# Optimization experiments

Measured on AMD Instinct MI355X. Metric: run time of the kernel, lower is better.

Reference implementation:

```python
import jax, jax.numpy as jnp
import numpy as np

B, S, IN, OUT = 4, 4096, 4096, 4096
N, R = 8, 64  # n_adapters, rank


def setup_inputs() -> dict:
    key = jax.random.key(0)
    ks = jax.random.split(key, 7)
    x = jax.random.normal(ks[0], (B, S, IN), dtype=jnp.float32)
    W = jax.random.normal(ks[1], (OUT, IN), dtype=jnp.float32) * 0.02
    b = jax.random.normal(ks[2], (OUT,), dtype=jnp.float32) * 0.02
    downs = jax.random.normal(ks[3], (N, R, IN), dtype=jnp.float32) * 0.02
    ups = jax.random.normal(ks[4], (N, OUT, R), dtype=jnp.float32) * 0.02
    mags = jax.random.uniform(ks[5], (N, OUT), dtype=jnp.float32)
    scales = jax.random.uniform(ks[6], (N,), dtype=jnp.float32)
    return {"x": x, "W": W, "b": b, "downs": downs, "ups": ups, "mags": mags, "scales": scales}


def reference(x, W, b, downs, ups, mags, scales):
    # Base linear: y = x @ W.T + b
    out = jnp.einsum("bsi,oi->bso", x, W) + b
    # All adapters batched: t[b,s,n,r] = x @ down_n.T
    t = jnp.einsum("bsi,nri->bsnr", x, downs)
    # Fold per-adapter DoRA magnitude and effective scale into the up proj:
    # delta = sum_n sc_n * mag_n * (t_n @ up_n.T)
    up_eff = ups * mags[:, :, None] * scales[:, None, None]  # [N, OUT, R]
    delta = jnp.einsum("bsnr,nor->bso", t, up_eff)
    return out + delta
```

## Files before the change

kernel.cpp:

```cpp
#include <hip/hip_runtime.h>


#define B_DIM 4
#define S_DIM 4096
#define IND   4096
#define OUTD  4096
#define NA    8
#define RK    64
#define MROWS (B_DIM * S_DIM)
#define KADAPT (NA * RK)

typedef __attribute__((ext_vector_type(8))) short short8;
typedef __attribute__((ext_vector_type(8))) unsigned short ushort8;
typedef __attribute__((ext_vector_type(4))) float float4v;

__device__ __forceinline__ unsigned short f2bf(float f) {
  unsigned int u = __builtin_bit_cast(unsigned int, f);
  u += 0x7FFFu + ((u >> 16) & 1u);
  return (unsigned short)(u >> 16);
}

__global__ void fold_up_k(const float* __restrict__ ups, const float* __restrict__ mags,
                          const float* __restrict__ scales, unsigned short* __restrict__ up_eff) {
  int tid = blockIdx.x * 256 + threadIdx.x;
  int o  = tid >> 9;
  int nr = tid & 511;
  int n  = nr >> 6;
  int r  = nr & 63;
  float v = ups[((size_t)n * OUTD + o) * RK + r] * mags[n * OUTD + o] * scales[n];
  up_eff[tid] = f2bf(v);
}

__global__ void tdown_k(const float* __restrict__ downs, unsigned short* __restrict__ dT) {
  int tid = blockIdx.x * 256 + threadIdx.x;
  int i  = tid >> 9;
  int nr = tid & 511;
  dT[tid] = f2bf(downs[(size_t)nr * IND + i]);
}

__global__ void cvt_x_k(const float* __restrict__ x, unsigned short* __restrict__ xb) {
  int tid = blockIdx.x * 256 + threadIdx.x;
  const float4v* xv = (const float4v*)x;
  float4v a = xv[2 * tid];
  float4v b = xv[2 * tid + 1];
  ushort8 o;
  o[0] = f2bf(a[0]); o[1] = f2bf(a[1]); o[2] = f2bf(a[2]); o[3] = f2bf(a[3]);
  o[4] = f2bf(b[0]); o[5] = f2bf(b[1]); o[6] = f2bf(b[2]); o[7] = f2bf(b[3]);
  ((ushort8*)xb)[tid] = o;
}

#define GLOAD_LDS16(g, l)                                                        \
  __builtin_amdgcn_global_load_lds((const __attribute__((address_space(1))) void*)(g), \
                                   (__attribute__((address_space(3))) void*)(l), 16, 0, 0)

template <int EPI>
__global__ __launch_bounds__(512, 2) void gemm256(const unsigned short* __restrict__ A,
                                                  const unsigned short* __restrict__ B,
                                                  const float* __restrict__ extra,
                                                  void* __restrict__ Cout,
                                                  int M, int N, int K) {
  __shared__ __align__(16) unsigned short As[2][2][256 * 32];
  __shared__ __align__(16) unsigned short Bs[2][2][256 * 32];

  const int tid  = threadIdx.x;
  const int lane = tid & 63;
  const int w    = tid >> 6;
  const int wm   = w >> 2;
  const int wn   = w & 3;
  const int qr   = lane & 15;
  const int ks   = (((lane >> 4) ^ ((qr >> 1) & 3))) * 8;

  const int nwg  = gridDim.x * gridDim.y;
  const int orig = blockIdx.y * gridDim.x + blockIdx.x;
  const int cpx  = nwg >> 3;
  const int swz  = (orig & 7) * cpx + (orig >> 3);
  const int bm   = swz / gridDim.y;
  const int bn   = swz % gridDim.y;

  const size_t Kz = (size_t)K;
  const int lrow = lane >> 2;
  const int lk   = (((lane & 3) ^ ((lrow >> 1) & 3))) * 8;
  const unsigned short* aSrc = A + ((size_t)bm * 256 + w * 32 + lrow) * Kz + lk;
  const unsigned short* bSrc = B + ((size_t)bn * 256 + w * 32 + lrow) * Kz + lk;
  const size_t seg1 = 16 * Kz;

  unsigned short* aBuf = &As[0][0][0];
  unsigned short* bBuf = &Bs[0][0][0];

#define STAGE(SRC, REG)                                 \
  do {                                                  \
    GLOAD_LDS16((SRC), (REG) + w * 1024);               \
    GLOAD_LDS16((SRC) + seg1, (REG) + w * 1024 + 512);  \
  } while (0)

#define LDS_A(REG, MH)                                                                    \
  {                                                                                       \
    _Pragma("unroll") for (int fm = 0; fm < 4; ++fm)                                      \
      a[fm] = *(const short8*)((REG) + (wm * 128 + ((MH) * 4 + fm) * 16 + qr) * 32 + ks); \
  }

#define LDS_B(REG)                                                                        \
  {                                                                                       \
    _Pragma("unroll") for (int fn = 0; fn < 4; ++fn)                                      \
      b[fn] = *(const short8*)((REG) + (wn * 64 + fn * 16 + qr) * 32 + ks);               \
  }

#define MFMA_Q(MH)                                                                        \
  __builtin_amdgcn_sched_barrier(0);                                                      \
  __builtin_amdgcn_s_barrier();                                                           \
  asm volatile("s_waitcnt lgkmcnt(0)" ::: "memory");                                      \
  __builtin_amdgcn_sched_barrier(0);                                                      \
  __builtin_amdgcn_s_setprio(1);                                                          \
  {                                                                                       \
    _Pragma("unroll") for (int fm = 0; fm < 4; ++fm)                                      \
      _Pragma("unroll") for (int fn = 0; fn < 4; ++fn)                                    \
        acc[(MH) * 4 + fm][fn] = __builtin_amdgcn_mfma_f32_16x16x32_bf16(                 \
            a[fm], b[fn], acc[(MH) * 4 + fm][fn], 0, 0, 0);                               \
  }                                                                                       \
  __builtin_amdgcn_s_setprio(0);                                                          \
  __builtin_amdgcn_sched_barrier(0);

  float4v acc[8][4] = {};
  short8 a[4], b[4];

  const int NT = K >> 6;

  STAGE(aSrc, aBuf);
  STAGE(bSrc, bBuf);
  STAGE(aSrc + 32, aBuf + 8192);
  STAGE(bSrc + 32, bBuf + 8192);
  asm volatile("s_waitcnt vmcnt(4)" ::: "memory");
  __builtin_amdgcn_s_barrier();

  for (int t = 0; t < NT - 1; ++t) {
    const int pc = (t & 1) << 14;
    const int pn = pc ^ 16384;
    unsigned short* aCur = aBuf + pc;
    unsigned short* bCur = bBuf + pc;
    unsigned short* aNx  = aBuf + pn;
    unsigned short* bNx  = bBuf + pn;
    const unsigned short* aN = aSrc + 64;
    const unsigned short* bN = bSrc + 64;

    LDS_A(aCur, 0);
    LDS_B(bCur);
    STAGE(aN, aNx);
    MFMA_Q(0);
    __builtin_amdgcn_s_barrier();

    LDS_A(aCur, 1);
    STAGE(bN, bNx);
    MFMA_Q(1);
    asm volatile("s_waitcnt vmcnt(4)" ::: "memory");
    __builtin_amdgcn_s_barrier();

    LDS_A(aCur + 8192, 0);
    LDS_B(bCur + 8192);
    STAGE(aN + 32, aNx + 8192);
    MFMA_Q(0);
    __builtin_amdgcn_s_barrier();

    LDS_A(aCur + 8192, 1);
    STAGE(bN + 32, bNx + 8192);
    MFMA_Q(1);
    asm volatile("s_waitcnt vmcnt(4)" ::: "memory");
    __builtin_amdgcn_s_barrier();

    aSrc = aN;
    bSrc = bN;
  }

  {
    const int pc = ((NT - 1) & 1) << 14;
    unsigned short* aCur = aBuf + pc;
    unsigned short* bCur = bBuf + pc;

    LDS_A(aCur, 0);
    LDS_B(bCur);
    MFMA_Q(0);
    __builtin_amdgcn_s_barrier();

    LDS_A(aCur, 1);
    MFMA_Q(1);
    asm volatile("s_waitcnt vmcnt(0)" ::: "memory");
    __builtin_amdgcn_s_barrier();

    LDS_A(aCur + 8192, 0);
    LDS_B(bCur + 8192);
    MFMA_Q(0);
    __builtin_amdgcn_s_barrier();

    LDS_A(aCur + 8192, 1);
    MFMA_Q(1);
  }

  if (EPI == 0) {
    float* C = (float*)Cout;
#pragma unroll
    for (int fn = 0; fn < 4; ++fn) {
      const int col = bn * 256 + wn * 64 + fn * 16 + qr;
      const float bias = extra[col];
#pragma unroll
      for (int fm = 0; fm < 8; ++fm) {
        const int rbase = bm * 256 + wm * 128 + fm * 16 + (lane >> 4) * 4;
#pragma unroll
        for (int r2 = 0; r2 < 4; ++r2)
          C[(size_t)(rbase + r2) * N + col] = acc[fm][fn][r2] + bias;
      }
    }
  } else {
    unsigned short* C = (unsigned short*)Cout;
#pragma unroll
    for (int fn = 0; fn < 4; ++fn) {
      const int col = bn * 256 + wn * 64 + fn * 16 + qr;
#pragma unroll
      for (int fm = 0; fm < 8; ++fm) {
        const int rbase = bm * 256 + wm * 128 + fm * 16 + (lane >> 4) * 4;
#pragma unroll
        for (int r2 = 0; r2 < 4; ++r2) {
          const size_t idx = (size_t)(rbase + r2) * N + col;
          C[idx] = f2bf(acc[fm][fn][r2] + extra[idx]);
        }
      }
    }
  }

#undef STAGE
#undef LDS_A
#undef LDS_B
#undef MFMA_Q
}

extern "C" void kernel_launch(void* const* d_in, const int* in_sizes, int n_in,
                              void* d_out, int out_size, void* d_ws, size_t ws_size,
                              hipStream_t stream) {
  const float* x      = (const float*)d_in[0];
  const float* W      = (const float*)d_in[1];
  const float* b      = (const float*)d_in[2];
  const float* downs  = (const float*)d_in[3];
  const float* ups    = (const float*)d_in[4];
  const float* mags   = (const float*)d_in[5];
  const float* scales = (const float*)d_in[6];
  float* out = (float*)d_out;

  char* ws = (char*)d_ws;
  unsigned short* x_bf   = (unsigned short*)ws;
  unsigned short* w_eff  = (unsigned short*)(ws + 134217728ull);
  unsigned short* up_eff = (unsigned short*)(ws + 134217728ull + 33554432ull);
  unsigned short* dT     = (unsigned short*)(ws + 134217728ull + 33554432ull + 4194304ull);

  fold_up_k<<<dim3((OUTD * KADAPT) / 256), dim3(256), 0, stream>>>(ups, mags, scales, up_eff);
  tdown_k<<<dim3((IND * KADAPT) / 256), dim3(256), 0, stream>>>(downs, dT);
  cvt_x_k<<<dim3((MROWS * IND / 8) / 256), dim3(256), 0, stream>>>(x, x_bf);

  gemm256<1><<<dim3(OUTD / 256, IND / 256), dim3(512), 0, stream>>>(
      up_eff, dT, W, (void*)w_eff, OUTD, IND, KADAPT);

  gemm256<0><<<dim3(MROWS / 256, OUTD / 256), dim3(512), 0, stream>>>(
      x_bf, w_eff, b, (void*)out, MROWS, OUTD, IND);
}
```

Measured before the change: 1.197 ms.

## Restructure GEMM main loop into simpler double-buffered tiles with register ping-pong

Replaces the hand-scheduled main loop, with its per-quarter barriers, waitcnts, sched_barriers and setprio, with a simpler TILE macro. The macro issues all four global-to-LDS stages for the next K tile up front, then reads A/B fragments into two register sets (a0/a1, b0/b1) interleaved with MFMAs, and ends with a single __syncthreads per tile. The loop is unrolled by two to alternate LDS buffers statically. This removes most explicit barriers and lets the compiler overlap LDS reads with MFMAs, at the cost of more register pressure. It also drops the explicit vmcnt waits, so the loop relies on __syncthreads to make the async LDS loads visible.

```diff
diff --git a/kernel.cpp b/kernel.cpp
--- a/kernel.cpp
+++ b/kernel.cpp
@@ -5,10 +5,10 @@
 #define S_DIM 4096
 #define IND   4096
 #define OUTD  4096
-#define NA    8
+#define NADP  8
 #define RK    64
 #define MROWS (B_DIM * S_DIM)
-#define KADAPT (NA * RK)
+#define KADAPT (NADP * RK)
 
 typedef __attribute__((ext_vector_type(8))) short short8;
 typedef __attribute__((ext_vector_type(8))) unsigned short ushort8;
@@ -84,115 +84,77 @@
   const unsigned short* bSrc = B + ((size_t)bn * 256 + w * 32 + lrow) * Kz + lk;
   const size_t seg1 = 16 * Kz;
 
-  unsigned short* aBuf = &As[0][0][0];
-  unsigned short* bBuf = &Bs[0][0][0];
-
-#define STAGE(SRC, REG)                                 \
+  unsigned short* aB = &As[0][0][0];
+  unsigned short* bB = &Bs[0][0][0];
+
+#define STAGE(SRC, DST)                                 \
   do {                                                  \
-    GLOAD_LDS16((SRC), (REG) + w * 1024);               \
-    GLOAD_LDS16((SRC) + seg1, (REG) + w * 1024 + 512);  \
+    GLOAD_LDS16((SRC), (DST) + w * 1024);               \
+    GLOAD_LDS16((SRC) + seg1, (DST) + w * 1024 + 512);  \
   } while (0)
 
-#define LDS_A(REG, MH)                                                                    \
+#define RD_A(DST, BUFP, MH, KSOFF)                                                        \
   {                                                                                       \
     _Pragma("unroll") for (int fm = 0; fm < 4; ++fm)                                      \
-      a[fm] = *(const short8*)((REG) + (wm * 128 + ((MH) * 4 + fm) * 16 + qr) * 32 + ks); \
-  }
-
-#define LDS_B(REG)                                                                        \
+      DST[fm] = *(const short8*)((BUFP) + (KSOFF) +                                       \
+                                 (wm * 128 + ((MH) * 4 + fm) * 16 + qr) * 32 + ks);       \
+  }
+
+#define RD_B(DST, BUFP, KSOFF)                                                            \
   {                                                                                       \
     _Pragma("unroll") for (int fn = 0; fn < 4; ++fn)                                      \
-      b[fn] = *(const short8*)((REG) + (wn * 64 + fn * 16 + qr) * 32 + ks);               \
-  }
-
-#define MFMA_Q(MH)                                                                        \
-  __builtin_amdgcn_sched_barrier(0);                                                      \
-  __builtin_amdgcn_s_barrier();                                                           \
-  asm volatile("s_waitcnt lgkmcnt(0)" ::: "memory");                                      \
-  __builtin_amdgcn_sched_barrier(0);                                                      \
-  __builtin_amdgcn_s_setprio(1);                                                          \
+      DST[fn] = *(const short8*)((BUFP) + (KSOFF) +                                       \
+                                 (wn * 64 + fn * 16 + qr) * 32 + ks);                     \
+  }
+
+#define MM(MH, AREG, BREG)                                                                \
   {                                                                                       \
     _Pragma("unroll") for (int fm = 0; fm < 4; ++fm)                                      \
       _Pragma("unroll") for (int fn = 0; fn < 4; ++fn)                                    \
         acc[(MH) * 4 + fm][fn] = __builtin_amdgcn_mfma_f32_16x16x32_bf16(                 \
-            a[fm], b[fn], acc[(MH) * 4 + fm][fn], 0, 0, 0);                               \
-  }                                                                                       \
-  __builtin_amdgcn_s_setprio(0);                                                          \
-  __builtin_amdgcn_sched_barrier(0);
+            AREG[fm], BREG[fn], acc[(MH) * 4 + fm][fn], 0, 0, 0);                         \
+  }
+
+#define TILE(CA, CB, NXA, NXB, DOSTAGE)                 \
+  do {                                                  \
+    if (DOSTAGE) {                                      \
+      STAGE(aSrc + 64, NXA);                            \
+      STAGE(bSrc + 64, NXB);                            \
+      STAGE(aSrc + 96, (NXA) + 8192);                   \
+      STAGE(bSrc + 96, (NXB) + 8192);                   \
+    }                                                   \
+    RD_A(a0, CA, 0, 0);                                 \
+    RD_B(b0, CB, 0);                                    \
+    RD_A(a1, CA, 1, 0);                                 \
+    MM(0, a0, b0);                                      \
+    RD_A(a0, CA, 0, 8192);                              \
+    RD_B(b1, CB, 8192);                                 \
+    MM(1, a1, b0);                                      \
+    RD_A(a1, CA, 1, 8192);                              \
+    MM(0, a0, b1);                                      \
+    MM(1, a1, b1);                                      \
+    __syncthreads();                                    \
+    aSrc += 64;                                         \
+    bSrc += 64;                                         \
+  } while (0)
 
   float4v acc[8][4] = {};
-  short8 a[4], b[4];
+  short8 a0[4], a1[4], b0[4], b1[4];
 
   const int NT = K >> 6;
 
-  STAGE(aSrc, aBuf);
-  STAGE(bSrc, bBuf);
-  STAGE(aSrc + 32, aBuf + 8192);
-  STAGE(bSrc + 32, bBuf + 8192);
-  asm volatile("s_waitcnt vmcnt(4)" ::: "memory");
-  __builtin_amdgcn_s_barrier();
-
-  for (int t = 0; t < NT - 1; ++t) {
-    const int pc = (t & 1) << 14;
-    const int pn = pc ^ 16384;
-    unsigned short* aCur = aBuf + pc;
-    unsigned short* bCur = bBuf + pc;
-    unsigned short* aNx  = aBuf + pn;
-    unsigned short* bNx  = bBuf + pn;
-    const unsigned short* aN = aSrc + 64;
-    const unsigned short* bN = bSrc + 64;
-
-    LDS_A(aCur, 0);
-    LDS_B(bCur);
-    STAGE(aN, aNx);
-    MFMA_Q(0);
-    __builtin_amdgcn_s_barrier();
-
-    LDS_A(aCur, 1);
-    STAGE(bN, bNx);
-    MFMA_Q(1);
-    asm volatile("s_waitcnt vmcnt(4)" ::: "memory");
-    __builtin_amdgcn_s_barrier();
-
-    LDS_A(aCur + 8192, 0);
-    LDS_B(bCur + 8192);
-    STAGE(aN + 32, aNx + 8192);
-    MFMA_Q(0);
-    __builtin_amdgcn_s_barrier();
-
-    LDS_A(aCur + 8192, 1);
-    STAGE(bN + 32, bNx + 8192);
-    MFMA_Q(1);
-    asm volatile("s_waitcnt vmcnt(4)" ::: "memory");
-    __builtin_amdgcn_s_barrier();
-
-    aSrc = aN;
-    bSrc = bN;
-  }
-
-  {
-    const int pc = ((NT - 1) & 1) << 14;
-    unsigned short* aCur = aBuf + pc;
-    unsigned short* bCur = bBuf + pc;
-
-    LDS_A(aCur, 0);
-    LDS_B(bCur);
-    MFMA_Q(0);
-    __builtin_amdgcn_s_barrier();
-
-    LDS_A(aCur, 1);
-    MFMA_Q(1);
-    asm volatile("s_waitcnt vmcnt(0)" ::: "memory");
-    __builtin_amdgcn_s_barrier();
-
-    LDS_A(aCur + 8192, 0);
-    LDS_B(bCur + 8192);
-    MFMA_Q(0);
-    __builtin_amdgcn_s_barrier();
-
-    LDS_A(aCur + 8192, 1);
-    MFMA_Q(1);
-  }
+  STAGE(aSrc, aB);
+  STAGE(bSrc, bB);
+  STAGE(aSrc + 32, aB + 8192);
+  STAGE(bSrc + 32, bB + 8192);
+  __syncthreads();
+
+  for (int t2 = 0; t2 < NT - 2; t2 += 2) {
+    TILE(aB,         bB,         aB + 16384, bB + 16384, true);
+    TILE(aB + 16384, bB + 16384, aB,         bB,         true);
+  }
+  TILE(aB,         bB,         aB + 16384, bB + 16384, true);
+  TILE(aB + 16384, bB + 16384, aB,         bB,         false);
 
   if (EPI == 0) {
     float* C = (float*)Cout;
@@ -226,9 +188,10 @@
   }
 
 #undef STAGE
-#undef LDS_A
-#undef LDS_B
-#undef MFMA_Q
+#undef RD_A
+#undef RD_B
+#undef MM
+#undef TILE
 }
 
 extern "C" void kernel_launch(void* const* d_in, const int* in_sizes, int n_in,
```

New measurement: 1.221 ms. No clear change (+2.0%).
